# Performance work log

Measured on AMD Instinct MI355X. Metric: run time of the kernel, lower is better.

## Reference

```python
import jax, jax.numpy as jnp
import numpy as np

EPS = 1e-06

def _feature_map(x):
    # elu(x) + 1, positive feature map
    return jax.nn.elu(x) + 1.0

def setup_inputs() -> dict:
    key = jax.random.key(0)
    k1, k2, k3 = jax.random.split(key, 3)
    B, L, d_k, d_v = 2, 4096, 128, 128
    Q = jax.random.normal(k1, (B, L, d_k), dtype=jnp.float32)
    K = jax.random.normal(k2, (B, L, d_k), dtype=jnp.float32)
    V = jax.random.normal(k3, (B, L, d_v), dtype=jnp.float32)
    return {"Q": Q, "K": K, "V": V}

def reference(Q, K, V):
    # Causal linear attention (ELU feature map).
    # out_l = phi(Q_l) @ sum_{j<=l} phi(K_j)^T V_j
    # Z_l   = phi(Q_l) . sum_{j<=l} phi(K_j)
    phiQ = _feature_map(Q)                       # (B, L, dk)
    phiK = _feature_map(K)                       # (B, L, dk)
    # cumulative KV state: (B, L, dk, dv) -- parallel replacement of the
    # original per-step bmm loop
    KV = jnp.cumsum(phiK[..., :, None] * V[..., None, :], axis=1)
    out = jnp.einsum('blk,blkv->blv', phiQ, KV)  # (B, L, dv)
    Kc = jnp.cumsum(phiK, axis=1)                # (B, L, dk)
    Z = jnp.einsum('blk,blk->bl', phiQ, Kc)[..., None]  # (B, L, 1)
    return out / (Z + EPS)
```

## Files before the change

### kernel.cpp

```cpp
#include <hip/hip_runtime.h>


#define EPS 1e-6f

constexpr int Bc = 2;
constexpr int L  = 4096;
constexpr int D  = 128;
constexpr int C  = 128;
constexpr int NC = L / C;
constexpr int P  = 136;

typedef short sh8 __attribute__((ext_vector_type(8)));
typedef float f4  __attribute__((ext_vector_type(4)));

__device__ __forceinline__ float phi(float x) {
    return x > 0.0f ? x + 1.0f : __expf(x);
}
__device__ __forceinline__ unsigned short f2bf(float f) {
    unsigned u = __float_as_uint(f);
    return (unsigned short)((u + 0x7FFFu + ((u >> 16) & 1u)) >> 16);
}
__device__ __forceinline__ float bf2f(unsigned short h) {
    return __uint_as_float(((unsigned)h) << 16);
}

__global__ __launch_bounds__(512) void k1(
    const float* __restrict__ K, const float* __restrict__ V,
    unsigned short* __restrict__ SB, float* __restrict__ Ksum) {
    const int c = blockIdx.x, b = blockIdx.y, vs = blockIdx.z;
    const int tid = threadIdx.x;
    __shared__ __align__(16) unsigned short sA[80 * P];
    __shared__ __align__(16) unsigned short sKb[128 * P];
    const size_t base = ((size_t)b * L + (size_t)c * C) * D;

    for (int k = 0; k < 4; ++k) {
        int fi = tid + 512 * k;
        int l = fi & 127, v4 = fi >> 7;
        float4 vd = *(const float4*)(V + base + (size_t)l * D + vs * 64 + v4 * 4);
        sA[(v4 * 4 + 0) * P + l] = f2bf(vd.x);
        sA[(v4 * 4 + 1) * P + l] = f2bf(vd.y);
        sA[(v4 * 4 + 2) * P + l] = f2bf(vd.z);
        sA[(v4 * 4 + 3) * P + l] = f2bf(vd.w);
    }
    for (int k = 0; k < 2; ++k) {
        int fi = tid + 512 * k;
        int row = fi >> 6, colp = fi & 63;
        *(unsigned*)(sA + (64 + row) * P + colp * 2) = (row == 0) ? 0x3F803F80u : 0u;
    }
    for (int k = 0; k < 8; ++k) {
        int fi = tid + 512 * k;
        int l = fi & 127, i4 = fi >> 7;
        float4 kd = *(const float4*)(K + base + (size_t)l * D + i4 * 4);
        sKb[(i4 * 4 + 0) * P + l] = f2bf(phi(kd.x));
        sKb[(i4 * 4 + 1) * P + l] = f2bf(phi(kd.y));
        sKb[(i4 * 4 + 2) * P + l] = f2bf(phi(kd.z));
        sKb[(i4 * 4 + 3) * P + l] = f2bf(phi(kd.w));
    }
    __syncthreads();

    const int w = tid >> 6, lane = tid & 63;
    const int r = lane & 15, q = lane >> 4;
    const int rbase = (w & 3) * 16;
    const int cbase = (w >> 2) * 64;
    const bool doZ = (vs == 0) && ((w & 3) == 0);

    f4 acc[4], kz[4];
#pragma unroll
    for (int f = 0; f < 4; ++f) { acc[f] = {0.f,0.f,0.f,0.f}; kz[f] = {0.f,0.f,0.f,0.f}; }
#pragma unroll
    for (int ks = 0; ks < 4; ++ks) {
        sh8 a  = *(const sh8*)(sA + (rbase + r) * P + ks * 32 + q * 8);
        sh8 az = *(const sh8*)(sA + (64 + r) * P + ks * 32 + q * 8);
#pragma unroll
        for (int f = 0; f < 4; ++f) {
            sh8 bb = *(const sh8*)(sKb + (cbase + f * 16 + r) * P + ks * 32 + q * 8);
            acc[f] = __builtin_amdgcn_mfma_f32_16x16x32_bf16(a, bb, acc[f], 0, 0, 0);
            if (doZ) kz[f] = __builtin_amdgcn_mfma_f32_16x16x32_bf16(az, bb, kz[f], 0, 0, 0);
        }
    }
    unsigned short* out = SB + ((size_t)(b * NC + c)) * D * D;
#pragma unroll
    for (int f = 0; f < 4; ++f) {
        int i = cbase + f * 16 + r;
#pragma unroll
        for (int e = 0; e < 4; ++e) {
            int v = vs * 64 + rbase + q * 4 + e;
            out[(size_t)v * D + i] = f2bf(acc[f][e]);
        }
    }
    if (doZ && q == 0) {
#pragma unroll
        for (int f = 0; f < 4; ++f)
            Ksum[((size_t)(b * NC + c)) * D + cbase + f * 16 + r] = kz[f][0];
    }
}

__global__ __launch_bounds__(256) void k_scan(unsigned short* __restrict__ SB,
                                              float* __restrict__ Ksum) {
    const int SD = D * D;
    int idx = blockIdx.x * 256 + threadIdx.x;
    if (idx < Bc * SD) {
        int b = idx / SD, e = idx % SD;
        float run = 0.0f;
        for (int c = 0; c < NC; ++c) {
            size_t off = ((size_t)(b * NC + c)) * SD + e;
            float t = bf2f(SB[off]);
            SB[off]  = f2bf(run);
            run += t;
        }
    } else if (idx < Bc * SD + Bc * D) {
        int rr = idx - Bc * SD;
        int b = rr >> 7, i = rr & 127;
        float run = 0.0f;
        for (int c = 0; c < NC; ++c) {
            size_t off = ((size_t)(b * NC + c)) * D + i;
            float t = Ksum[off];
            Ksum[off] = run;
            run += t;
        }
    }
}

__global__ __launch_bounds__(512) void k_out(
    const float* __restrict__ Q, const float* __restrict__ K,
    const float* __restrict__ V, const unsigned short* __restrict__ SB,
    const float* __restrict__ Ksum, float* __restrict__ Out) {
    const int c = blockIdx.x, b = blockIdx.y, rs = blockIdx.z;
    const int tid = threadIdx.x;
    __shared__ __align__(16) unsigned short sQ[32 * P];
    __shared__ __align__(16) unsigned short sKb[144 * P];
    __shared__ __align__(16) unsigned short sV[144 * P];
    __shared__ __align__(16) unsigned short sAm[32 * P];
    __shared__ float sZ[32];
    const size_t base  = ((size_t)b * L + (size_t)c * C) * D;
    const size_t qbase = base + (size_t)rs * 32 * D;

    for (int k = 0; k < 2; ++k) {
        int fi = tid + 512 * k;
        int row = fi >> 5, c4 = fi & 31;
        float4 qd = *(const float4*)(Q + qbase + (size_t)row * D + c4 * 4);
        uint2 pk;
        pk.x = (unsigned)f2bf(phi(qd.x)) | ((unsigned)f2bf(phi(qd.y)) << 16);
        pk.y = (unsigned)f2bf(phi(qd.z)) | ((unsigned)f2bf(phi(qd.w)) << 16);
        *(uint2*)(sQ + row * P + c4 * 4) = pk;
    }
    for (int k = 0; k < 8; ++k) {
        int fi = tid + 512 * k;
        int row = fi >> 5, c4 = fi & 31;
        float4 kd = *(const float4*)(K + base + (size_t)row * D + c4 * 4);
        uint2 pk;
        pk.x = (unsigned)f2bf(phi(kd.x)) | ((unsigned)f2bf(phi(kd.y)) << 16);
        pk.y = (unsigned)f2bf(phi(kd.z)) | ((unsigned)f2bf(phi(kd.w)) << 16);
        *(uint2*)(sKb + row * P + c4 * 4) = pk;
    }
    for (int k = 0; k < 8; ++k) {
        int fi = tid + 512 * k;
        int j = fi & 127, v4 = fi >> 7;
        float4 vd = *(const float4*)(V + base + (size_t)j * D + v4 * 4);
        sV[(v4 * 4 + 0) * P + j] = f2bf(vd.x);
        sV[(v4 * 4 + 1) * P + j] = f2bf(vd.y);
        sV[(v4 * 4 + 2) * P + j] = f2bf(vd.z);
        sV[(v4 * 4 + 3) * P + j] = f2bf(vd.w);
    }
    for (int k = 0; k < 2; ++k) {
        int fi = tid + 512 * k;
        int row = fi >> 6, colp = fi & 63;
        *(unsigned*)(sV + (128 + row) * P + colp * 2) = (row == 0) ? 0x3F803F80u : 0u;
    }
    __syncthreads();

    const int w = tid >> 6, lane = tid & 63;
    const int r = lane & 15, q = lane >> 4;
    const int rbase = (w & 1) * 16;
    const int cq = w >> 1, cbase = cq * 32;
    const bool doZ = (cq == 3);

    f4 a2[2];
#pragma unroll
    for (int f = 0; f < 2; ++f) a2[f] = {0.f,0.f,0.f,0.f};
#pragma unroll
    for (int ks = 0; ks < 4; ++ks) {
        sh8 a = *(const sh8*)(sQ + (rbase + r) * P + ks * 32 + q * 8);
#pragma unroll
        for (int f = 0; f < 2; ++f) {
            sh8 bb = *(const sh8*)(sKb + (cbase + f * 16 + r) * P + ks * 32 + q * 8);
            a2[f] = __builtin_amdgcn_mfma_f32_16x16x32_bf16(a, bb, a2[f], 0, 0, 0);
        }
    }
#pragma unroll
    for (int f = 0; f < 2; ++f) {
        int j = cbase + f * 16 + r;
#pragma unroll
        for (int e = 0; e < 4; ++e) {
            int lr = rbase + q * 4 + e;
            sAm[lr * P + j] = f2bf((j <= rs * 32 + lr) ? a2[f][e] : 0.0f);
        }
    }
    __syncthreads();

    {
        const uint4* sbg = (const uint4*)(SB + ((size_t)(b * NC + c)) * D * D);
        for (int k = 0; k < 4; ++k) {
            int fi = tid + 512 * k;
            int v = fi >> 4, ch = fi & 15;
            uint4 dd = sbg[fi];
            *(uint4*)(sKb + v * P + ch * 8) = dd;
        }
        if (tid < 32) {
            float4 kq = ((const float4*)(Ksum + ((size_t)(b * NC + c)) * D))[tid];
            uint2 pk;
            pk.x = (unsigned)f2bf(kq.x) | ((unsigned)f2bf(kq.y) << 16);
            pk.y = (unsigned)f2bf(kq.z) | ((unsigned)f2bf(kq.w) << 16);
            *(uint2*)(sKb + 128 * P + tid * 4) = pk;
        }
        for (int k = 0; k < 2; ++k) {
            int fi = tid + 512 * k;
            if (fi < 960) {
                int row = 129 + (fi >> 6), colp = fi & 63;
                *(unsigned*)(sKb + row * P + colp * 2) = 0u;
            }
        }
    }

    f4 acc[2], zacc = {0.f,0.f,0.f,0.f};
#pragma unroll
    for (int f = 0; f < 2; ++f) acc[f] = {0.f,0.f,0.f,0.f};
#pragma unroll
    for (int ks = 0; ks < 4; ++ks) {
        sh8 a = *(const sh8*)(sAm + (rbase + r) * P + ks * 32 + q * 8);
#pragma unroll
        for (int f = 0; f < 2; ++f) {
            sh8 bb = *(const sh8*)(sV + (cbase + f * 16 + r) * P + ks * 32 + q * 8);
            acc[f] = __builtin_amdgcn_mfma_f32_16x16x32_bf16(a, bb, acc[f], 0, 0, 0);
        }
        if (doZ) {
            sh8 bz = *(const sh8*)(sV + (128 + r) * P + ks * 32 + q * 8);
            zacc = __builtin_amdgcn_mfma_f32_16x16x32_bf16(a, bz, zacc, 0, 0, 0);
        }
    }
    __syncthreads();

#pragma unroll
    for (int ks = 0; ks < 4; ++ks) {
        sh8 a = *(const sh8*)(sQ + (rbase + r) * P + ks * 32 + q * 8);
#pragma unroll
        for (int f = 0; f < 2; ++f) {
            sh8 bb = *(const sh8*)(sKb + (cbase + f * 16 + r) * P + ks * 32 + q * 8);
            acc[f] = __builtin_amdgcn_mfma_f32_16x16x32_bf16(a, bb, acc[f], 0, 0, 0);
        }
        if (doZ) {
            sh8 bz = *(const sh8*)(sKb + (128 + r) * P + ks * 32 + q * 8);
            zacc = __builtin_amdgcn_mfma_f32_16x16x32_bf16(a, bz, zacc, 0, 0, 0);
        }
    }
    if (doZ && r == 0) {
#pragma unroll
        for (int e = 0; e < 4; ++e) sZ[rbase + q * 4 + e] = zacc[e] + EPS;
    }
    __syncthreads();

#pragma unroll
    for (int f = 0; f < 2; ++f) {
        int v = cbase + f * 16 + r;
#pragma unroll
        for (int e = 0; e < 4; ++e) {
            int lr = rbase + q * 4 + e;
            Out[base + (size_t)(rs * 32 + lr) * D + v] = acc[f][e] / sZ[lr];
        }
    }
}

extern "C" void kernel_launch(void* const* d_in, const int* in_sizes, int n_in,
                              void* d_out, int out_size, void* d_ws, size_t ws_size,
                              hipStream_t stream) {
    const float* Q = (const float*)d_in[0];
    const float* K = (const float*)d_in[1];
    const float* V = (const float*)d_in[2];
    float* Out = (float*)d_out;
    unsigned short* SBw = (unsigned short*)d_ws;
    float* Ksum = (float*)((char*)d_ws + (size_t)Bc * NC * D * D * 2);

    k1<<<dim3(NC, Bc, 2), 512, 0, stream>>>(K, V, SBw, Ksum);
    int total = Bc * D * D + Bc * D;
    k_scan<<<dim3((total + 255) / 256), 256, 0, stream>>>(SBw, Ksum);
    k_out<<<dim3(NC, Bc, 4), 512, 0, stream>>>(Q, K, V, SBw, Ksum, Out);
}
```

Baseline: 80.67 us.

## Add prep kernel precomputing bf16 phi(Q/K) and transposed K/V tiles

Adds a new k_prep kernel that applies the feature map once, converts Q, K and V to bf16, and writes both row-major and per-chunk transposed copies to workspace. k1 and k_out then load these pre-packed tiles with wide 16-byte copies instead of re-reading fp32 inputs and doing scattered transposed LDS stores. The all-ones rows used for the normaliser are replaced with register splats, and the Ksum operand is read straight into registers. The scan kernel now loads all chunk values before writing them back. The cost is an extra launch and extra workspace traffic for the bf16 intermediates.

```diff
diff --git a/kernel.cpp b/kernel.cpp
--- a/kernel.cpp
+++ b/kernel.cpp
@@ -23,38 +23,98 @@
 __device__ __forceinline__ float bf2f(unsigned short h) {
     return __uint_as_float(((unsigned)h) << 16);
 }
+__device__ __forceinline__ sh8 splat1() {
+    sh8 s;
+#pragma unroll
+    for (int j = 0; j < 8; ++j) s[j] = (short)0x3F80;
+    return s;
+}
+
+__global__ __launch_bounds__(512) void k_prep(
+    const float* __restrict__ Q, const float* __restrict__ K,
+    const float* __restrict__ V,
+    unsigned short* __restrict__ QB, unsigned short* __restrict__ KB,
+    unsigned short* __restrict__ KT, unsigned short* __restrict__ VT) {
+    const int c = blockIdx.x, b = blockIdx.y, zz = blockIdx.z;
+    const int tid = threadIdx.x;
+    __shared__ __align__(16) unsigned short sT[128 * P];
+    const size_t base  = ((size_t)b * L + (size_t)c * C) * D;
+    const size_t tbase = ((size_t)(b * NC + c)) * D * D;
+
+    if (zz == 0) {
+        for (int k = 0; k < 8; ++k) {
+            int fi = tid + 512 * k;
+            int l = fi >> 5, i4 = fi & 31;
+            float4 d = *(const float4*)(K + base + (size_t)l * D + i4 * 4);
+            unsigned short e0 = f2bf(phi(d.x)), e1 = f2bf(phi(d.y));
+            unsigned short e2 = f2bf(phi(d.z)), e3 = f2bf(phi(d.w));
+            uint2 pk;
+            pk.x = (unsigned)e0 | ((unsigned)e1 << 16);
+            pk.y = (unsigned)e2 | ((unsigned)e3 << 16);
+            *(uint2*)(KB + base + (size_t)l * D + i4 * 4) = pk;
+            int blk = (((l >> 3) + i4) & 15) * 8 + (l & 7);
+            sT[(i4 * 4 + 0) * P + blk] = e0;
+            sT[(i4 * 4 + 1) * P + blk] = e1;
+            sT[(i4 * 4 + 2) * P + blk] = e2;
+            sT[(i4 * 4 + 3) * P + blk] = e3;
+        }
+        __syncthreads();
+        for (int k = 0; k < 4; ++k) {
+            int fi = tid + 512 * k;
+            int i = fi >> 4, lch = fi & 15;
+            uint4 dd = *(const uint4*)(sT + i * P + (((lch + (i >> 2)) & 15) * 8));
+            *(uint4*)(KT + tbase + (size_t)i * D + lch * 8) = dd;
+        }
+    } else {
+        for (int k = 0; k < 8; ++k) {
+            int fi = tid + 512 * k;
+            int l = fi >> 5, i4 = fi & 31;
+            float4 d = *(const float4*)(V + base + (size_t)l * D + i4 * 4);
+            int blk = (((l >> 3) + i4) & 15) * 8 + (l & 7);
+            sT[(i4 * 4 + 0) * P + blk] = f2bf(d.x);
+            sT[(i4 * 4 + 1) * P + blk] = f2bf(d.y);
+            sT[(i4 * 4 + 2) * P + blk] = f2bf(d.z);
+            sT[(i4 * 4 + 3) * P + blk] = f2bf(d.w);
+        }
+        for (int k = 0; k < 8; ++k) {
+            int fi = tid + 512 * k;
+            int l = fi >> 5, i4 = fi & 31;
+            float4 d = *(const float4*)(Q + base + (size_t)l * D + i4 * 4);
+            uint2 pk;
+            pk.x = (unsigned)f2bf(phi(d.x)) | ((unsigned)f2bf(phi(d.y)) << 16);
+            pk.y = (unsigned)f2bf(phi(d.z)) | ((unsigned)f2bf(phi(d.w)) << 16);
+            *(uint2*)(QB + base + (size_t)l * D + i4 * 4) = pk;
+        }
+        __syncthreads();
+        for (int k = 0; k < 4; ++k) {
+            int fi = tid + 512 * k;
+            int v = fi >> 4, lch = fi & 15;
+            uint4 dd = *(const uint4*)(sT + v * P + (((lch + (v >> 2)) & 15) * 8));
+            *(uint4*)(VT + tbase + (size_t)v * D + lch * 8) = dd;
+        }
+    }
+}
 
 __global__ __launch_bounds__(512) void k1(
-    const float* __restrict__ K, const float* __restrict__ V,
+    const unsigned short* __restrict__ KT, const unsigned short* __restrict__ VT,
     unsigned short* __restrict__ SB, float* __restrict__ Ksum) {
     const int c = blockIdx.x, b = blockIdx.y, vs = blockIdx.z;
     const int tid = threadIdx.x;
-    __shared__ __align__(16) unsigned short sA[80 * P];
+    __shared__ __align__(16) unsigned short sA[64 * P];
     __shared__ __align__(16) unsigned short sKb[128 * P];
-    const size_t base = ((size_t)b * L + (size_t)c * C) * D;
-
+    const size_t tbase = ((size_t)(b * NC + c)) * D * D;
+
+    const uint4* vtg = (const uint4*)(VT + tbase + (size_t)vs * 64 * D);
+    for (int k = 0; k < 2; ++k) {
+        int fi = tid + 512 * k;
+        int v = fi >> 4, ch = fi & 15;
+        *(uint4*)(sA + v * P + ch * 8) = vtg[fi];
+    }
+    const uint4* ktg = (const uint4*)(KT + tbase);
     for (int k = 0; k < 4; ++k) {
         int fi = tid + 512 * k;
-        int l = fi & 127, v4 = fi >> 7;
-        float4 vd = *(const float4*)(V + base + (size_t)l * D + vs * 64 + v4 * 4);
-        sA[(v4 * 4 + 0) * P + l] = f2bf(vd.x);
-        sA[(v4 * 4 + 1) * P + l] = f2bf(vd.y);
-        sA[(v4 * 4 + 2) * P + l] = f2bf(vd.z);
-        sA[(v4 * 4 + 3) * P + l] = f2bf(vd.w);
-    }
-    for (int k = 0; k < 2; ++k) {
-        int fi = tid + 512 * k;
-        int row = fi >> 6, colp = fi & 63;
-        *(unsigned*)(sA + (64 + row) * P + colp * 2) = (row == 0) ? 0x3F803F80u : 0u;
-    }
-    for (int k = 0; k < 8; ++k) {
-        int fi = tid + 512 * k;
-        int l = fi & 127, i4 = fi >> 7;
-        float4 kd = *(const float4*)(K + base + (size_t)l * D + i4 * 4);
-        sKb[(i4 * 4 + 0) * P + l] = f2bf(phi(kd.x));
-        sKb[(i4 * 4 + 1) * P + l] = f2bf(phi(kd.y));
-        sKb[(i4 * 4 + 2) * P + l] = f2bf(phi(kd.z));
-        sKb[(i4 * 4 + 3) * P + l] = f2bf(phi(kd.w));
+        int i = fi >> 4, ch = fi & 15;
+        *(uint4*)(sKb + i * P + ch * 8) = ktg[fi];
     }
     __syncthreads();
 
@@ -63,14 +123,14 @@
     const int rbase = (w & 3) * 16;
     const int cbase = (w >> 2) * 64;
     const bool doZ = (vs == 0) && ((w & 3) == 0);
+    const sh8 az = splat1();
 
     f4 acc[4], kz[4];
 #pragma unroll
     for (int f = 0; f < 4; ++f) { acc[f] = {0.f,0.f,0.f,0.f}; kz[f] = {0.f,0.f,0.f,0.f}; }
 #pragma unroll
     for (int ks = 0; ks < 4; ++ks) {
-        sh8 a  = *(const sh8*)(sA + (rbase + r) * P + ks * 32 + q * 8);
-        sh8 az = *(const sh8*)(sA + (64 + r) * P + ks * 32 + q * 8);
+        sh8 a = *(const sh8*)(sA + (rbase + r) * P + ks * 32 + q * 8);
 #pragma unroll
         for (int f = 0; f < 4; ++f) {
             sh8 bb = *(const sh8*)(sKb + (cbase + f * 16 + r) * P + ks * 32 + q * 8);
@@ -78,7 +138,7 @@
             if (doZ) kz[f] = __builtin_amdgcn_mfma_f32_16x16x32_bf16(az, bb, kz[f], 0, 0, 0);
         }
     }
-    unsigned short* out = SB + ((size_t)(b * NC + c)) * D * D;
+    unsigned short* out = SB + tbase;
 #pragma unroll
     for (int f = 0; f < 4; ++f) {
         int i = cbase + f * 16 + r;
@@ -101,71 +161,61 @@
     int idx = blockIdx.x * 256 + threadIdx.x;
     if (idx < Bc * SD) {
         int b = idx / SD, e = idx % SD;
+        size_t off0 = (size_t)b * NC * SD + e;
+        unsigned short vals[NC];
+#pragma unroll
+        for (int c = 0; c < NC; ++c) vals[c] = SB[off0 + (size_t)c * SD];
         float run = 0.0f;
+#pragma unroll
         for (int c = 0; c < NC; ++c) {
-            size_t off = ((size_t)(b * NC + c)) * SD + e;
-            float t = bf2f(SB[off]);
-            SB[off]  = f2bf(run);
-            run += t;
+            SB[off0 + (size_t)c * SD] = f2bf(run);
+            run += bf2f(vals[c]);
         }
     } else if (idx < Bc * SD + Bc * D) {
         int rr = idx - Bc * SD;
         int b = rr >> 7, i = rr & 127;
+        size_t off0 = (size_t)b * NC * D + i;
+        float vals[NC];
+#pragma unroll
+        for (int c = 0; c < NC; ++c) vals[c] = Ksum[off0 + (size_t)c * D];
         float run = 0.0f;
+#pragma unroll
         for (int c = 0; c < NC; ++c) {
-            size_t off = ((size_t)(b * NC + c)) * D + i;
-            float t = Ksum[off];
-            Ksum[off] = run;
-            run += t;
+            Ksum[off0 + (size_t)c * D] = run;
+            run += vals[c];
         }
     }
 }
 
 __global__ __launch_bounds__(512) void k_out(
-    const float* __restrict__ Q, const float* __restrict__ K,
-    const float* __restrict__ V, const unsigned short* __restrict__ SB,
+    const unsigned short* __restrict__ QB, const unsigned short* __restrict__ KB,
+    const unsigned short* __restrict__ VT, const unsigned short* __restrict__ SB,
     const float* __restrict__ Ksum, float* __restrict__ Out) {
     const int c = blockIdx.x, b = blockIdx.y, rs = blockIdx.z;
     const int tid = threadIdx.x;
     __shared__ __align__(16) unsigned short sQ[32 * P];
-    __shared__ __align__(16) unsigned short sKb[144 * P];
-    __shared__ __align__(16) unsigned short sV[144 * P];
+    __shared__ __align__(16) unsigned short sKb[128 * P];
+    __shared__ __align__(16) unsigned short sV[128 * P];
     __shared__ __align__(16) unsigned short sAm[32 * P];
     __shared__ float sZ[32];
     const size_t base  = ((size_t)b * L + (size_t)c * C) * D;
-    const size_t qbase = base + (size_t)rs * 32 * D;
-
-    for (int k = 0; k < 2; ++k) {
-        int fi = tid + 512 * k;
-        int row = fi >> 5, c4 = fi & 31;
-        float4 qd = *(const float4*)(Q + qbase + (size_t)row * D + c4 * 4);
-        uint2 pk;
-        pk.x = (unsigned)f2bf(phi(qd.x)) | ((unsigned)f2bf(phi(qd.y)) << 16);
-        pk.y = (unsigned)f2bf(phi(qd.z)) | ((unsigned)f2bf(phi(qd.w)) << 16);
-        *(uint2*)(sQ + row * P + c4 * 4) = pk;
-    }
-    for (int k = 0; k < 8; ++k) {
-        int fi = tid + 512 * k;
-        int row = fi >> 5, c4 = fi & 31;
-        float4 kd = *(const float4*)(K + base + (size_t)row * D + c4 * 4);
-        uint2 pk;
-        pk.x = (unsigned)f2bf(phi(kd.x)) | ((unsigned)f2bf(phi(kd.y)) << 16);
-        pk.y = (unsigned)f2bf(phi(kd.z)) | ((unsigned)f2bf(phi(kd.w)) << 16);
-        *(uint2*)(sKb + row * P + c4 * 4) = pk;
-    }
-    for (int k = 0; k < 8; ++k) {
-        int fi = tid + 512 * k;
-        int j = fi & 127, v4 = fi >> 7;
-        float4 vd = *(const float4*)(V + base + (size_t)j * D + v4 * 4);
-        sV[(v4 * 4 + 0) * P + j] = f2bf(vd.x);
-        sV[(v4 * 4 + 1) * P + j] = f2bf(vd.y);
-        sV[(v4 * 4 + 2) * P + j] = f2bf(vd.z);
-        sV[(v4 * 4 + 3) * P + j] = f2bf(vd.w);
-    }
-    for (int k = 0; k < 2; ++k) {
-        int fi = tid + 512 * k;
-        int row = fi >> 6, colp = fi & 63;
-        *(unsigned*)(sV + (128 + row) * P + colp * 2) = (row == 0) ? 0x3F803F80u : 0u;
+    const size_t tbase = ((size_t)(b * NC + c)) * D * D;
+    const size_t kb    = ((size_t)(b * NC + c)) * D;
+
+    {
+        const uint4* qg = (const uint4*)(QB + base + (size_t)rs * 32 * D);
+        int fi = tid;
+        *(uint4*)(sQ + (fi >> 4) * P + (fi & 15) * 8) = qg[fi];
+        const uint4* kg = (const uint4*)(KB + base);
+        for (int k = 0; k < 4; ++k) {
+            int f2 = tid + 512 * k;
+            *(uint4*)(sKb + (f2 >> 4) * P + (f2 & 15) * 8) = kg[f2];
+        }
+        const uint4* vg = (const uint4*)(VT + tbase);
+        for (int k = 0; k < 4; ++k) {
+            int f2 = tid + 512 * k;
+            *(uint4*)(sV + (f2 >> 4) * P + (f2 & 15) * 8) = vg[f2];
+        }
     }
     __syncthreads();
 
@@ -175,6 +225,21 @@
     const int cq = w >> 1, cbase = cq * 32;
     const bool doZ = (cq == 3);
 
+    sh8 bzk[4];
+    if (doZ) {
+#pragma unroll
+        for (int ks = 0; ks < 4; ++ks) {
+            float4 f0 = *(const float4*)(Ksum + kb + ks * 32 + q * 8);
+            float4 f1 = *(const float4*)(Ksum + kb + ks * 32 + q * 8 + 4);
+            sh8 t;
+            t[0] = (short)f2bf(f0.x); t[1] = (short)f2bf(f0.y);
+            t[2] = (short)f2bf(f0.z); t[3] = (short)f2bf(f0.w);
+            t[4] = (short)f2bf(f1.x); t[5] = (short)f2bf(f1.y);
+            t[6] = (short)f2bf(f1.z); t[7] = (short)f2bf(f1.w);
+            bzk[ks] = t;
+        }
+    }
+
     f4 a2[2];
 #pragma unroll
     for (int f = 0; f < 2; ++f) a2[f] = {0.f,0.f,0.f,0.f};
@@ -199,32 +264,17 @@
     __syncthreads();
 
     {
-        const uint4* sbg = (const uint4*)(SB + ((size_t)(b * NC + c)) * D * D);
-        for (int k = 0; k < 4; ++k) {
-            int fi = tid + 512 * k;
-            int v = fi >> 4, ch = fi & 15;
-            uint4 dd = sbg[fi];
-            *(uint4*)(sKb + v * P + ch * 8) = dd;
-        }
-        if (tid < 32) {
-            float4 kq = ((const float4*)(Ksum + ((size_t)(b * NC + c)) * D))[tid];
-            uint2 pk;
-            pk.x = (unsigned)f2bf(kq.x) | ((unsigned)f2bf(kq.y) << 16);
-            pk.y = (unsigned)f2bf(kq.z) | ((unsigned)f2bf(kq.w) << 16);
-            *(uint2*)(sKb + 128 * P + tid * 4) = pk;
-        }
-        for (int k = 0; k < 2; ++k) {
-            int fi = tid + 512 * k;
-            if (fi < 960) {
-                int row = 129 + (fi >> 6), colp = fi & 63;
-                *(unsigned*)(sKb + row * P + colp * 2) = 0u;
-            }
+        const uint4* sg = (const uint4*)(SB + tbase);
+        for (int k = 0; k < 4; ++k) {
+            int f2 = tid + 512 * k;
+            *(uint4*)(sKb + (f2 >> 4) * P + (f2 & 15) * 8) = sg[f2];
         }
     }
 
     f4 acc[2], zacc = {0.f,0.f,0.f,0.f};
 #pragma unroll
     for (int f = 0; f < 2; ++f) acc[f] = {0.f,0.f,0.f,0.f};
+    const sh8 bones = splat1();
 #pragma unroll
     for (int ks = 0; ks < 4; ++ks) {
         sh8 a = *(const sh8*)(sAm + (rbase + r) * P + ks * 32 + q * 8);
@@ -233,10 +283,7 @@
             sh8 bb = *(const sh8*)(sV + (cbase + f * 16 + r) * P + ks * 32 + q * 8);
             acc[f] = __builtin_amdgcn_mfma_f32_16x16x32_bf16(a, bb, acc[f], 0, 0, 0);
         }
-        if (doZ) {
-            sh8 bz = *(const sh8*)(sV + (128 + r) * P + ks * 32 + q * 8);
-            zacc = __builtin_amdgcn_mfma_f32_16x16x32_bf16(a, bz, zacc, 0, 0, 0);
-        }
+        if (doZ) zacc = __builtin_amdgcn_mfma_f32_16x16x32_bf16(a, bones, zacc, 0, 0, 0);
     }
     __syncthreads();
 
@@ -248,10 +295,7 @@
             sh8 bb = *(const sh8*)(sKb + (cbase + f * 16 + r) * P + ks * 32 + q * 8);
             acc[f] = __builtin_amdgcn_mfma_f32_16x16x32_bf16(a, bb, acc[f], 0, 0, 0);
         }
-        if (doZ) {
-            sh8 bz = *(const sh8*)(sKb + (128 + r) * P + ks * 32 + q * 8);
-            zacc = __builtin_amdgcn_mfma_f32_16x16x32_bf16(a, bz, zacc, 0, 0, 0);
-        }
+        if (doZ) zacc = __builtin_amdgcn_mfma_f32_16x16x32_bf16(a, bzk[ks], zacc, 0, 0, 0);
     }
     if (doZ && r == 0) {
 #pragma unroll
@@ -277,11 +321,18 @@
     const float* K = (const float*)d_in[1];
     const float* V = (const float*)d_in[2];
     float* Out = (float*)d_out;
-    unsigned short* SBw = (unsigned short*)d_ws;
-    float* Ksum = (float*)((char*)d_ws + (size_t)Bc * NC * D * D * 2);
-
-    k1<<<dim3(NC, Bc, 2), 512, 0, stream>>>(K, V, SBw, Ksum);
+    constexpr size_t NE = (size_t)Bc * L * D;
+    char* w = (char*)d_ws;
+    unsigned short* SBw  = (unsigned short*)(w);
+    float*          Ksum = (float*)(w + NE * 2);
+    unsigned short* QB   = (unsigned short*)(w + NE * 2 + (size_t)Bc * NC * D * 4);
+    unsigned short* KB   = QB + NE;
+    unsigned short* KT   = KB + NE;
+    unsigned short* VT   = KT + NE;
+
+    k_prep<<<dim3(NC, Bc, 2), 512, 0, stream>>>(Q, K, V, QB, KB, KT, VT);
+    k1<<<dim3(NC, Bc, 2), 512, 0, stream>>>(KT, VT, SBw, Ksum);
     int total = Bc * D * D + Bc * D;
     k_scan<<<dim3((total + 255) / 256), 256, 0, stream>>>(SBw, Ksum);
-    k_out<<<dim3(NC, Bc, 4), 512, 0, stream>>>(Q, K, V, SBw, Ksum, Out);
-}
+    k_out<<<dim3(NC, Bc, 4), 512, 0, stream>>>(QB, KB, VT, SBw, Ksum, Out);
+}
```

New measurement: 82.20 us. About the same (+1.9%).
